# Optimization experiments

Hardware: AMD Instinct MI355X
Metric: run time of the kernel (lower is better)

## Reference

```python
import jax, jax.numpy as jnp
import numpy as np

N_ENT = 50000
N_REL = 16
D_E = 64
D_R = 64
D_OUT = 32
N_EDGE = 1000000


def setup_inputs() -> dict:
    key = jax.random.key(0)
    ks = jax.random.split(key, 8)
    # 0.1 scale keeps tanh / softmax in a realistic (non-saturated) range,
    # mimicking trained embedding magnitudes.
    entity_table = jax.random.normal(ks[0], (N_ENT, D_E), dtype=jnp.float32) * 0.1
    relation_table = jax.random.normal(ks[1], (N_REL, D_R), dtype=jnp.float32) * 0.1
    W_R = jax.random.normal(ks[2], (N_REL, D_E, D_R), dtype=jnp.float32) * (1.0 / np.sqrt(D_E))
    W1 = jax.random.normal(ks[3], (D_E, D_OUT), dtype=jnp.float32) * (1.0 / np.sqrt(D_E))
    b1 = jnp.zeros((D_OUT,), dtype=jnp.float32)
    W2 = jax.random.normal(ks[4], (D_E, D_OUT), dtype=jnp.float32) * (1.0 / np.sqrt(D_E))
    b2 = jnp.zeros((D_OUT,), dtype=jnp.float32)
    src = jax.random.randint(ks[5], (N_EDGE,), 0, N_ENT, dtype=jnp.int32)
    dst = jax.random.randint(ks[6], (N_EDGE,), 0, N_ENT, dtype=jnp.int32)
    etype = jax.random.randint(ks[7], (N_EDGE,), 0, N_REL, dtype=jnp.int32)
    return {"entity_table": entity_table, "relation_table": relation_table,
            "W_R": W_R, "W1": W1, "b1": b1, "W2": W2, "b2": b2,
            "src": src, "dst": dst, "etype": etype}


def reference(entity_table, relation_table, W_R, W1, b1, W2, b2, src, dst, etype):
    """KGAT calc_att (per-relation edge attention + edge softmax) followed by
    one bi-interaction Aggregator layer (dropout = identity, eval mode)."""
    n_nodes = entity_table.shape[0]
    # Per-relation projection of all node embeddings (grouped GEMM form of the
    # per-relation loop in compute_attention): [R, N, d_r]
    proj = jnp.einsum('nd,rde->rne', entity_table, W_R)
    r_mul_h = proj[etype, src]            # [E, d_r]  h W_r per edge
    r_mul_t = proj[etype, dst]            # [E, d_r]  t W_r per edge
    r_e = relation_table[etype]           # [E, d_r]
    # att = (h W_r) . tanh(t W_r + r)
    att = jnp.sum(r_mul_h * jnp.tanh(r_mul_t + r_e), axis=-1)  # [E]
    # edge softmax grouped by destination node
    att_max = jax.ops.segment_max(att, dst, num_segments=n_nodes)     # [N]
    ex = jnp.exp(att - att_max[dst])
    denom = jax.ops.segment_sum(ex, dst, num_segments=n_nodes)        # [N]
    a = ex / denom[dst]                                               # [E]
    # u_mul_e + sum: N_h[v] = sum_{(u->v)} a_e * node[u]
    msg = a[:, None] * entity_table[src]                              # [E, d]
    N_h = jax.ops.segment_sum(msg, dst, num_segments=n_nodes)         # [N, d]
    node = entity_table
    # bi-interaction aggregator (LeakyReLU slope 0.01, torch default)
    out1 = jax.nn.leaky_relu((node + N_h) @ W1 + b1)
    out2 = jax.nn.leaky_relu((node * N_h) @ W2 + b2)
    return out1 + out2
```

## Files before the change

kernel.cpp:

```cpp
#include <hip/hip_runtime.h>
#include <math.h>

#define NREL 16
#define DE 64
#define DOUT 32
#define NPART 8

typedef __attribute__((ext_vector_type(8))) short bf16x8;
typedef __attribute__((ext_vector_type(16))) float f32x16;

__device__ __forceinline__ short f2bf(float f) {
    unsigned u = __builtin_bit_cast(unsigned, f);
    unsigned r = (u + 0x7FFFu + ((u >> 16) & 1u)) >> 16;
    return (short)r;
}
__device__ __forceinline__ float bf2f(short s) {
    unsigned u = ((unsigned)(unsigned short)s) << 16;
    return __builtin_bit_cast(float, u);
}
__device__ __forceinline__ unsigned cvt_pk_bf16(float lo, float hi) {
    unsigned r;
    asm("v_cvt_pk_bf16_f32 %0, %1, %2" : "=v"(r) : "v"(lo), "v"(hi));
    return r;
}
__device__ __forceinline__ float tanh_fast(float x) {
    float e = __expf(2.0f * x);
    return fmaf(-2.0f, __builtin_amdgcn_rcpf(e + 1.0f), 1.0f);
}

__global__ __launch_bounds__(256) void hist_kernel(const int* __restrict__ dst,
                                                   int* __restrict__ counts,
                                                   int E, int psz) {
    int part = blockIdx.x & (NPART - 1);
    int i = (blockIdx.x >> 3) * 256 + threadIdx.x;
    if (i < E) {
        int d = dst[i];
        if (d >= part * psz && d < (part + 1) * psz)
            atomicAdd(&counts[d], 1);
    }
}

__global__ __launch_bounds__(256) void blocksum_kernel(const int* __restrict__ counts,
                                                       int* __restrict__ blockSums, int n) {
    __shared__ int wsum[4];
    int i = blockIdx.x * 256 + threadIdx.x;
    int v = (i < n) ? counts[i] : 0;
#pragma unroll
    for (int off = 1; off < 64; off <<= 1) v += __shfl_xor(v, off);
    if ((threadIdx.x & 63) == 0) wsum[threadIdx.x >> 6] = v;
    __syncthreads();
    if (threadIdx.x == 0)
        blockSums[blockIdx.x] = wsum[0] + wsum[1] + wsum[2] + wsum[3];
}

__global__ __launch_bounds__(1024) void blockscan_kernel(int* __restrict__ blockSums, int nb) {
    __shared__ int lds[1024];
    int t = threadIdx.x;
    int v = (t < nb) ? blockSums[t] : 0;
    lds[t] = v;
    __syncthreads();
    for (int off = 1; off < 1024; off <<= 1) {
        int u = (t >= off) ? lds[t - off] : 0;
        __syncthreads();
        lds[t] += u;
        __syncthreads();
    }
    if (t < nb) blockSums[t] = (t == 0) ? 0 : lds[t - 1];
}

__global__ __launch_bounds__(256) void scanout_kernel(const int* __restrict__ counts,
                                                      const int* __restrict__ blockSums,
                                                      int* __restrict__ offsets,
                                                      int* __restrict__ cursor, int n) {
    __shared__ int wsum[4];
    int t = threadIdx.x;
    int i = blockIdx.x * 256 + t;
    int lane = t & 63;
    int w = t >> 6;
    int v = (i < n) ? counts[i] : 0;
    int incl = v;
#pragma unroll
    for (int off = 1; off < 64; off <<= 1) {
        int u = __shfl_up(incl, off);
        if (lane >= off) incl += u;
    }
    if (lane == 63) wsum[w] = incl;
    __syncthreads();
    int woff = 0;
#pragma unroll
    for (int j = 0; j < 4; ++j) if (j < w) woff += wsum[j];
    int excl = incl - v + woff + blockSums[blockIdx.x];
    if (i < n) { offsets[i] = excl; cursor[i] = excl; }
    if (i == n - 1) offsets[n] = excl + v;
}

__global__ __launch_bounds__(256) void scatter_kernel(const int* __restrict__ dst,
                                                      const int* __restrict__ src,
                                                      const int* __restrict__ etype,
                                                      int* __restrict__ cursor,
                                                      int* __restrict__ pks,
                                                      int E, int psz) {
    int part = blockIdx.x & (NPART - 1);
    int i = (blockIdx.x >> 3) * 256 + threadIdx.x;
    if (i < E) {
        int d = dst[i];
        if (d >= part * psz && d < (part + 1) * psz) {
            int pos = atomicAdd(&cursor[d], 1);
            pks[pos] = (src[i] << 4) | etype[i];
        }
    }
}

__global__ __launch_bounds__(256) void entcvt_kernel(const float* __restrict__ ent,
                                                     short* __restrict__ entbf, int tot) {
    int i = blockIdx.x * 256 + threadIdx.x;
    if (i < tot) entbf[i] = f2bf(ent[i]);
}

__global__ __launch_bounds__(256) void wcvt_kernel(const float* __restrict__ WR,
                                                   short* __restrict__ Wbf,
                                                   short* __restrict__ WTbf) {
    int i = blockIdx.x * 256 + threadIdx.x;
    int r = i >> 12, k = (i >> 6) & 63, j = i & 63;
    short b = f2bf(WR[i]);
    Wbf[i] = b;
    WTbf[(r << 12) + (j << 6) + k] = b;
}

#define TQ 392
__global__ __launch_bounds__(256) void projq_kernel(const short* __restrict__ entbf,
                                                    const float* __restrict__ rel,
                                                    const short* __restrict__ Wbf,
                                                    const short* __restrict__ WTbf,
                                                    short* __restrict__ Qbf, int N) {
    __shared__ short Tl[4 * 2048];
    int lane = threadIdx.x & 63;
    int wid = threadIdx.x >> 6;
    int lin = blockIdx.x;
    int r = lin / TQ;
    int tq = lin - r * TQ;
    int m0 = (tq * 4 + wid) * 32;
    if (m0 >= N) return;
    int hi = lane >> 5;
    int lo = lane & 31;

    int arow = m0 + lo;
    if (arow >= N) arow = N - 1;
    const short* ap = entbf + ((size_t)arow << 6) + hi * 8;
    bf16x8 A[4];
#pragma unroll
    for (int kk = 0; kk < 4; ++kk) A[kk] = *(const bf16x8*)(ap + kk * 16);

    short* tb = Tl + wid * 2048;
    const short* wtb = WTbf + ((size_t)r << 12);
    const short* wb  = Wbf  + ((size_t)r << 12);

    f32x16 acc0 = {}, acc1 = {};
#pragma unroll
    for (int kk = 0; kk < 4; ++kk) {
        bf16x8 b0 = *(const bf16x8*)(wtb + lo * DE + kk * 16 + hi * 8);
        bf16x8 b1 = *(const bf16x8*)(wtb + (lo + 32) * DE + kk * 16 + hi * 8);
        acc0 = __builtin_amdgcn_mfma_f32_32x32x16_bf16(A[kk], b0, acc0, 0, 0, 0);
        acc1 = __builtin_amdgcn_mfma_f32_32x32x16_bf16(A[kk], b1, acc1, 0, 0, 0);
    }
    float rv0 = rel[r * DE + lo];
    float rv1 = rel[r * DE + 32 + lo];
#pragma unroll
    for (int i = 0; i < 16; ++i) {
        int row = (i & 3) + 8 * (i >> 2) + 4 * hi;
        int sw = (row & 7) << 3;
        unsigned u = cvt_pk_bf16(tanh_fast(acc0[i] + rv0), tanh_fast(acc1[i] + rv1));
        tb[(row * DE + lo) ^ sw] = (short)(u & 0xffff);
        tb[(row * DE + 32 + lo) ^ sw] = (short)(u >> 16);
    }
    bf16x8 A2[4];
#pragma unroll
    for (int kk = 0; kk < 4; ++kk)
        A2[kk] = *(const bf16x8*)(tb + ((lo * DE + kk * 16 + hi * 8) ^ ((lo & 7) << 3)));

    f32x16 q0 = {}, q1 = {};
#pragma unroll
    for (int kk = 0; kk < 4; ++kk) {
        bf16x8 b0 = *(const bf16x8*)(wb + lo * DE + kk * 16 + hi * 8);
        bf16x8 b1 = *(const bf16x8*)(wb + (lo + 32) * DE + kk * 16 + hi * 8);
        q0 = __builtin_amdgcn_mfma_f32_32x32x16_bf16(A2[kk], b0, q0, 0, 0, 0);
        q1 = __builtin_amdgcn_mfma_f32_32x32x16_bf16(A2[kk], b1, q1, 0, 0, 0);
    }
#pragma unroll
    for (int i = 0; i < 16; ++i) {
        int row = (i & 3) + 8 * (i >> 2) + 4 * hi;
        unsigned u = cvt_pk_bf16(q0[i], q1[i]);
        tb[row * DE + lo] = (short)(u & 0xffff);
        tb[row * DE + 32 + lo] = (short)(u >> 16);
    }
#pragma unroll
    for (int p = 0; p < 4; ++p) {
        int row = p * 8 + (lane >> 3);
        int node = m0 + row;
        bf16x8 vq = *(const bf16x8*)(tb + row * DE + (lane & 7) * 8);
        if (node < N)
            *(bf16x8*)(Qbf + (((size_t)r * N + node) << 6) + (lane & 7) * 8) = vq;
    }
}

__global__ __launch_bounds__(256) void agg_kernel(const float* __restrict__ ent,
                                                  const short* __restrict__ entbf,
                                                  const short* __restrict__ Qbf,
                                                  const int* __restrict__ offsets,
                                                  const int* __restrict__ pks,
                                                  const float* __restrict__ W1,
                                                  const float* __restrict__ b1,
                                                  const float* __restrict__ W2,
                                                  const float* __restrict__ b2,
                                                  float* __restrict__ out, int n) {
    __shared__ float xl[4][128];
    int lane = threadIdx.x & 63;
    int wid = threadIdx.x >> 6;
    int v = (blockIdx.x << 2) + wid;
    if (v >= n) return;
    int o0 = offsets[v], o1 = offsets[v + 1];
    int g = lane >> 3, gl = lane & 7;
    const short* qbase = Qbf + ((size_t)v << 6) + gl * 8;

    float m = -INFINITY, l = 0.f;
    float acc[8];
#pragma unroll
    for (int j = 0; j < 8; ++j) acc[j] = 0.f;

    int k = o0 + g;
    bool val = k < o1;
    bf16x8 xv = {}, qv = {};
    if (val) {
        int pk = pks[k];
        xv = *(const bf16x8*)(entbf + ((size_t)(pk >> 4) << 6) + gl * 8);
        qv = *(const bf16x8*)(qbase + (((unsigned)(pk & 15) * (unsigned)n) << 6));
    }
    int iters = (o1 - o0 + 7) >> 3;
    for (int it = 0; it < iters; ++it) {
        int kn = k + 8;
        bool valn = kn < o1;
        bf16x8 xn = {}, qn = {};
        if (valn) {
            int pk = pks[kn];
            xn = *(const bf16x8*)(entbf + ((size_t)(pk >> 4) << 6) + gl * 8);
            qn = *(const bf16x8*)(qbase + (((unsigned)(pk & 15) * (unsigned)n) << 6));
        }
        float xf[8];
        float d = 0.f;
#pragma unroll
        for (int j = 0; j < 8; ++j) {
            xf[j] = bf2f(xv[j]);
            d = fmaf(xf[j], bf2f(qv[j]), d);
        }
        d += __shfl_xor(d, 1);
        d += __shfl_xor(d, 2);
        d += __shfl_xor(d, 4);
        float p = val ? d : -INFINITY;
        float nm = fmaxf(m, p);
        float sc, pe;
        if (nm == -INFINITY) { sc = 0.f; pe = 0.f; }
        else { sc = __expf(m - nm); pe = __expf(p - nm); }
        l = l * sc + pe;
#pragma unroll
        for (int j = 0; j < 8; ++j) acc[j] = fmaf(acc[j], sc, pe * xf[j]);
        m = nm;
        k = kn; val = valn; xv = xn; qv = qn;
    }
#pragma unroll
    for (int off = 8; off < 64; off <<= 1) {
        float mo = __shfl_xor(m, off);
        float lo2 = __shfl_xor(l, off);
        float nm = fmaxf(m, mo);
        float s1 = (nm == -INFINITY) ? 0.f : __expf(m - nm);
        float s2 = (nm == -INFINITY) ? 0.f : __expf(mo - nm);
        l = l * s1 + lo2 * s2;
#pragma unroll
        for (int j = 0; j < 8; ++j) {
            float ao = __shfl_xor(acc[j], off);
            acc[j] = acc[j] * s1 + ao * s2;
        }
        m = nm;
    }
    float* xw = &xl[wid][0];
    float invl = (l > 0.f) ? (1.0f / l) : 0.f;
    if (g == 0) {
#pragma unroll
        for (int j = 0; j < 8; ++j) xw[gl * 8 + j] = acc[j] * invl;
    }
    float node = ent[((size_t)v << 6) + lane];
    float Nh = xw[lane];
    float x1 = node + Nh;
    float x2 = node * Nh;
    xw[lane] = x1;
    xw[64 + lane] = x2;
    int j = lane & 31;
    const float* __restrict__ Wsel = (lane < 32) ? W1 : W2;
    float bias = (lane < 32) ? b1[j] : b2[j];
    const float* xb = xw + ((lane < 32) ? 0 : 64);
    float o = 0.f;
#pragma unroll 8
    for (int kk = 0; kk < DE; ++kk)
        o = fmaf(xb[kk], Wsel[kk * DOUT + j], o);
    o += bias;
    float lr = (o > 0.f) ? o : 0.01f * o;
    float other = __shfl_xor(lr, 32);
    if (lane < 32) out[(size_t)v * DOUT + lane] = lr + other;
}

extern "C" void kernel_launch(void* const* d_in, const int* in_sizes, int n_in,
                              void* d_out, int out_size, void* d_ws, size_t ws_size,
                              hipStream_t stream) {
    const float* ent = (const float*)d_in[0];
    const float* rel = (const float*)d_in[1];
    const float* WR  = (const float*)d_in[2];
    const float* W1  = (const float*)d_in[3];
    const float* b1  = (const float*)d_in[4];
    const float* W2  = (const float*)d_in[5];
    const float* b2  = (const float*)d_in[6];
    const int* src   = (const int*)d_in[7];
    const int* dst   = (const int*)d_in[8];
    const int* ety   = (const int*)d_in[9];
    float* out       = (float*)d_out;

    const int E = in_sizes[7];
    const int N = in_sizes[0] / DE;
    const int NB = (N + 255) / 256;
    const int psz = (N + NPART - 1) / NPART;
    const int chunks = (E + 255) / 256;

    size_t qElems  = (size_t)N * NREL * DE;
    size_t eElems  = (size_t)N * DE;
    size_t wElems  = (size_t)NREL * DE * DE;

    char* ws = (char*)d_ws;
    short* Qbf   = (short*)ws;
    short* entbf = Qbf + qElems;
    short* Wbf   = entbf + eElems;
    short* WTbf  = Wbf + wElems;
    int* counts  = (int*)(WTbf + wElems);
    int* offsets = counts + N;
    int* cursor  = offsets + N + 1;
    int* pks     = cursor + N;
    int* bsums   = pks + E;
    size_t need  = (size_t)((char*)(bsums + NB) - ws);
    if (ws_size < need) return;

    hipMemsetAsync(counts, 0, (size_t)N * 4, stream);
    entcvt_kernel<<<(int)((eElems + 255) / 256), 256, 0, stream>>>(ent, entbf, (int)eElems);
    wcvt_kernel<<<(int)(wElems / 256), 256, 0, stream>>>(WR, Wbf, WTbf);
    hist_kernel<<<chunks * NPART, 256, 0, stream>>>(dst, counts, E, psz);
    blocksum_kernel<<<NB, 256, 0, stream>>>(counts, bsums, N);
    blockscan_kernel<<<1, 1024, 0, stream>>>(bsums, NB);
    scanout_kernel<<<NB, 256, 0, stream>>>(counts, bsums, offsets, cursor, N);
    scatter_kernel<<<chunks * NPART, 256, 0, stream>>>(dst, src, ety, cursor, pks, E, psz);
    projq_kernel<<<TQ * NREL, 256, 0, stream>>>(entbf, rel, Wbf, WTbf, Qbf, N);
    agg_kernel<<<(N + 3) / 4, 256, 0, stream>>>(ent, entbf, Qbf, offsets, pks,
                                                W1, b1, W2, b2, out, N);
}
```

Measured before the change: 236.2 us.

## Store projected Q table in FP8 and merge small kernels into fused launches

The per-relation projected table Q is now written as FP8 bytes instead of bf16, halving the bytes gathered per edge in the aggregation kernel, which decodes them with packed fp8-to-f32 conversions. The entity/weight conversion and histogram kernels are merged into one launch, and the scatter kernel is merged with the projection kernel so the two independent workloads share a grid. This cuts launch count and gather bandwidth, at the cost of lower precision in the attention logits and some extra per-element conversion instructions.

Measured after the change: 222.1 us. 1.06x faster.

```diff
diff --git a/kernel.cpp b/kernel.cpp
--- a/kernel.cpp
+++ b/kernel.cpp
@@ -5,9 +5,11 @@
 #define DE 64
 #define DOUT 32
 #define NPART 8
+#define TQ 392
 
 typedef __attribute__((ext_vector_type(8))) short bf16x8;
 typedef __attribute__((ext_vector_type(16))) float f32x16;
+typedef __attribute__((ext_vector_type(2))) float f32x2;
 
 __device__ __forceinline__ short f2bf(float f) {
     unsigned u = __builtin_bit_cast(unsigned, f);
@@ -18,25 +20,43 @@
     unsigned u = ((unsigned)(unsigned short)s) << 16;
     return __builtin_bit_cast(float, u);
 }
-__device__ __forceinline__ unsigned cvt_pk_bf16(float lo, float hi) {
-    unsigned r;
-    asm("v_cvt_pk_bf16_f32 %0, %1, %2" : "=v"(r) : "v"(lo), "v"(hi));
-    return r;
+__device__ __forceinline__ unsigned char f2fp8(float f) {
+    int p = __builtin_amdgcn_cvt_pk_fp8_f32(f, f, 0, false);
+    return (unsigned char)(p & 0xff);
 }
 __device__ __forceinline__ float tanh_fast(float x) {
     float e = __expf(2.0f * x);
     return fmaf(-2.0f, __builtin_amdgcn_rcpf(e + 1.0f), 1.0f);
 }
 
-__global__ __launch_bounds__(256) void hist_kernel(const int* __restrict__ dst,
+__global__ __launch_bounds__(256) void prep_kernel(const float* __restrict__ ent,
+                                                   short* __restrict__ entbf, int eTot,
+                                                   const float* __restrict__ WR,
+                                                   short* __restrict__ Wbf,
+                                                   short* __restrict__ WTbf,
+                                                   const int* __restrict__ dst,
                                                    int* __restrict__ counts,
-                                                   int E, int psz) {
-    int part = blockIdx.x & (NPART - 1);
-    int i = (blockIdx.x >> 3) * 256 + threadIdx.x;
-    if (i < E) {
-        int d = dst[i];
-        if (d >= part * psz && d < (part + 1) * psz)
-            atomicAdd(&counts[d], 1);
+                                                   int E, int psz,
+                                                   int eB, int wB) {
+    int b = blockIdx.x;
+    if (b < eB) {
+        int i = b * 256 + threadIdx.x;
+        if (i < eTot) entbf[i] = f2bf(ent[i]);
+    } else if (b < eB + wB) {
+        int i = (b - eB) * 256 + threadIdx.x;
+        int r = i >> 12, k = (i >> 6) & 63, j = i & 63;
+        short w = f2bf(WR[i]);
+        Wbf[i] = w;
+        WTbf[(r << 12) + (j << 6) + k] = w;
+    } else {
+        int hb = b - eB - wB;
+        int part = hb & (NPART - 1);
+        int i = (hb >> 3) * 256 + threadIdx.x;
+        if (i < E) {
+            int d = dst[i];
+            if (d >= part * psz && d < (part + 1) * psz)
+                atomicAdd(&counts[d], 1);
+        }
     }
 }
 
@@ -94,46 +114,32 @@
     if (i == n - 1) offsets[n] = excl + v;
 }
 
-__global__ __launch_bounds__(256) void scatter_kernel(const int* __restrict__ dst,
-                                                      const int* __restrict__ src,
-                                                      const int* __restrict__ etype,
-                                                      int* __restrict__ cursor,
-                                                      int* __restrict__ pks,
-                                                      int E, int psz) {
-    int part = blockIdx.x & (NPART - 1);
-    int i = (blockIdx.x >> 3) * 256 + threadIdx.x;
-    if (i < E) {
-        int d = dst[i];
-        if (d >= part * psz && d < (part + 1) * psz) {
-            int pos = atomicAdd(&cursor[d], 1);
-            pks[pos] = (src[i] << 4) | etype[i];
-        }
-    }
-}
-
-__global__ __launch_bounds__(256) void entcvt_kernel(const float* __restrict__ ent,
-                                                     short* __restrict__ entbf, int tot) {
-    int i = blockIdx.x * 256 + threadIdx.x;
-    if (i < tot) entbf[i] = f2bf(ent[i]);
-}
-
-__global__ __launch_bounds__(256) void wcvt_kernel(const float* __restrict__ WR,
-                                                   short* __restrict__ Wbf,
-                                                   short* __restrict__ WTbf) {
-    int i = blockIdx.x * 256 + threadIdx.x;
-    int r = i >> 12, k = (i >> 6) & 63, j = i & 63;
-    short b = f2bf(WR[i]);
-    Wbf[i] = b;
-    WTbf[(r << 12) + (j << 6) + k] = b;
-}
-
-#define TQ 392
-__global__ __launch_bounds__(256) void projq_kernel(const short* __restrict__ entbf,
-                                                    const float* __restrict__ rel,
-                                                    const short* __restrict__ Wbf,
-                                                    const short* __restrict__ WTbf,
-                                                    short* __restrict__ Qbf, int N) {
+__global__ __launch_bounds__(256) void projscat_kernel(const short* __restrict__ entbf,
+                                                       const float* __restrict__ rel,
+                                                       const short* __restrict__ Wbf,
+                                                       const short* __restrict__ WTbf,
+                                                       unsigned char* __restrict__ Qf8,
+                                                       int N, int nProj,
+                                                       const int* __restrict__ dst,
+                                                       const int* __restrict__ src,
+                                                       const int* __restrict__ etype,
+                                                       int* __restrict__ cursor,
+                                                       int* __restrict__ pks,
+                                                       int E, int psz) {
     __shared__ short Tl[4 * 2048];
+    if ((int)blockIdx.x >= nProj) {
+        int sb = blockIdx.x - nProj;
+        int part = sb & (NPART - 1);
+        int i = (sb >> 3) * 256 + threadIdx.x;
+        if (i < E) {
+            int d = dst[i];
+            if (d >= part * psz && d < (part + 1) * psz) {
+                int pos = atomicAdd(&cursor[d], 1);
+                pks[pos] = (src[i] << 4) | etype[i];
+            }
+        }
+        return;
+    }
     int lane = threadIdx.x & 63;
     int wid = threadIdx.x >> 6;
     int lin = blockIdx.x;
@@ -169,9 +175,8 @@
     for (int i = 0; i < 16; ++i) {
         int row = (i & 3) + 8 * (i >> 2) + 4 * hi;
         int sw = (row & 7) << 3;
-        unsigned u = cvt_pk_bf16(tanh_fast(acc0[i] + rv0), tanh_fast(acc1[i] + rv1));
-        tb[(row * DE + lo) ^ sw] = (short)(u & 0xffff);
-        tb[(row * DE + 32 + lo) ^ sw] = (short)(u >> 16);
+        tb[(row * DE + lo) ^ sw] = f2bf(tanh_fast(acc0[i] + rv0));
+        tb[(row * DE + 32 + lo) ^ sw] = f2bf(tanh_fast(acc1[i] + rv1));
     }
     bf16x8 A2[4];
 #pragma unroll
@@ -186,26 +191,26 @@
         q0 = __builtin_amdgcn_mfma_f32_32x32x16_bf16(A2[kk], b0, q0, 0, 0, 0);
         q1 = __builtin_amdgcn_mfma_f32_32x32x16_bf16(A2[kk], b1, q1, 0, 0, 0);
     }
+    unsigned char* tb8 = (unsigned char*)tb;
 #pragma unroll
     for (int i = 0; i < 16; ++i) {
         int row = (i & 3) + 8 * (i >> 2) + 4 * hi;
-        unsigned u = cvt_pk_bf16(q0[i], q1[i]);
-        tb[row * DE + lo] = (short)(u & 0xffff);
-        tb[row * DE + 32 + lo] = (short)(u >> 16);
+        tb8[row * DE + lo] = f2fp8(q0[i]);
+        tb8[row * DE + 32 + lo] = f2fp8(q1[i]);
     }
 #pragma unroll
     for (int p = 0; p < 4; ++p) {
         int row = p * 8 + (lane >> 3);
         int node = m0 + row;
-        bf16x8 vq = *(const bf16x8*)(tb + row * DE + (lane & 7) * 8);
+        unsigned long long vq = *(const unsigned long long*)(tb8 + row * DE + (lane & 7) * 8);
         if (node < N)
-            *(bf16x8*)(Qbf + (((size_t)r * N + node) << 6) + (lane & 7) * 8) = vq;
+            *(unsigned long long*)(Qf8 + (((size_t)r * N + node) << 6) + (lane & 7) * 8) = vq;
     }
 }
 
 __global__ __launch_bounds__(256) void agg_kernel(const float* __restrict__ ent,
                                                   const short* __restrict__ entbf,
-                                                  const short* __restrict__ Qbf,
+                                                  const unsigned char* __restrict__ Qf8,
                                                   const int* __restrict__ offsets,
                                                   const int* __restrict__ pks,
                                                   const float* __restrict__ W1,
@@ -220,7 +225,7 @@
     if (v >= n) return;
     int o0 = offsets[v], o1 = offsets[v + 1];
     int g = lane >> 3, gl = lane & 7;
-    const short* qbase = Qbf + ((size_t)v << 6) + gl * 8;
+    const unsigned char* qbase = Qf8 + ((size_t)v << 6) + gl * 8;
 
     float m = -INFINITY, l = 0.f;
     float acc[8];
@@ -229,28 +234,35 @@
 
     int k = o0 + g;
     bool val = k < o1;
-    bf16x8 xv = {}, qv = {};
+    bf16x8 xv = {};
+    uint2 qv = {};
     if (val) {
         int pk = pks[k];
         xv = *(const bf16x8*)(entbf + ((size_t)(pk >> 4) << 6) + gl * 8);
-        qv = *(const bf16x8*)(qbase + (((unsigned)(pk & 15) * (unsigned)n) << 6));
+        qv = *(const uint2*)(qbase + (((size_t)(pk & 15) * (size_t)n) << 6));
     }
     int iters = (o1 - o0 + 7) >> 3;
     for (int it = 0; it < iters; ++it) {
         int kn = k + 8;
         bool valn = kn < o1;
-        bf16x8 xn = {}, qn = {};
+        bf16x8 xn = {};
+        uint2 qn = {};
         if (valn) {
             int pk = pks[kn];
             xn = *(const bf16x8*)(entbf + ((size_t)(pk >> 4) << 6) + gl * 8);
-            qn = *(const bf16x8*)(qbase + (((unsigned)(pk & 15) * (unsigned)n) << 6));
-        }
+            qn = *(const uint2*)(qbase + (((size_t)(pk & 15) * (size_t)n) << 6));
+        }
+        f32x2 qa = __builtin_amdgcn_cvt_pk_f32_fp8(qv.x, false);
+        f32x2 qb = __builtin_amdgcn_cvt_pk_f32_fp8(qv.x, true);
+        f32x2 qc = __builtin_amdgcn_cvt_pk_f32_fp8(qv.y, false);
+        f32x2 qd = __builtin_amdgcn_cvt_pk_f32_fp8(qv.y, true);
+        float qf[8] = {qa[0], qa[1], qb[0], qb[1], qc[0], qc[1], qd[0], qd[1]};
         float xf[8];
         float d = 0.f;
 #pragma unroll
         for (int j = 0; j < 8; ++j) {
             xf[j] = bf2f(xv[j]);
-            d = fmaf(xf[j], bf2f(qv[j]), d);
+            d = fmaf(xf[j], qf[j], d);
         }
         d += __shfl_xor(d, 1);
         d += __shfl_xor(d, 2);
@@ -328,13 +340,13 @@
     const int psz = (N + NPART - 1) / NPART;
     const int chunks = (E + 255) / 256;
 
-    size_t qElems  = (size_t)N * NREL * DE;
+    size_t qBytes  = (size_t)N * NREL * DE;
     size_t eElems  = (size_t)N * DE;
     size_t wElems  = (size_t)NREL * DE * DE;
 
     char* ws = (char*)d_ws;
-    short* Qbf   = (short*)ws;
-    short* entbf = Qbf + qElems;
+    unsigned char* Qf8 = (unsigned char*)ws;
+    short* entbf = (short*)(ws + qBytes);
     short* Wbf   = entbf + eElems;
     short* WTbf  = Wbf + wElems;
     int* counts  = (int*)(WTbf + wElems);
@@ -345,15 +357,18 @@
     size_t need  = (size_t)((char*)(bsums + NB) - ws);
     if (ws_size < need) return;
 
+    const int eB = (int)((eElems + 255) / 256);
+    const int wB = (int)(wElems / 256);
+    const int nProj = TQ * NREL;
+
     hipMemsetAsync(counts, 0, (size_t)N * 4, stream);
-    entcvt_kernel<<<(int)((eElems + 255) / 256), 256, 0, stream>>>(ent, entbf, (int)eElems);
-    wcvt_kernel<<<(int)(wElems / 256), 256, 0, stream>>>(WR, Wbf, WTbf);
-    hist_kernel<<<chunks * NPART, 256, 0, stream>>>(dst, counts, E, psz);
+    prep_kernel<<<eB + wB + chunks * NPART, 256, 0, stream>>>(
+        ent, entbf, (int)eElems, WR, Wbf, WTbf, dst, counts, E, psz, eB, wB);
     blocksum_kernel<<<NB, 256, 0, stream>>>(counts, bsums, N);
     blockscan_kernel<<<1, 1024, 0, stream>>>(bsums, NB);
     scanout_kernel<<<NB, 256, 0, stream>>>(counts, bsums, offsets, cursor, N);
-    scatter_kernel<<<chunks * NPART, 256, 0, stream>>>(dst, src, ety, cursor, pks, E, psz);
-    projq_kernel<<<TQ * NREL, 256, 0, stream>>>(entbf, rel, Wbf, WTbf, Qbf, N);
-    agg_kernel<<<(N + 3) / 4, 256, 0, stream>>>(ent, entbf, Qbf, offsets, pks,
+    projscat_kernel<<<nProj + chunks * NPART, 256, 0, stream>>>(
+        entbf, rel, Wbf, WTbf, Qf8, N, nProj, dst, src, ety, cursor, pks, E, psz);
+    agg_kernel<<<(N + 3) / 4, 256, 0, stream>>>(ent, entbf, Qf8, offsets, pks,
                                                 W1, b1, W2, b2, out, N);
 }
```
